# Performance work log

Hardware: AMD Instinct MI355X
Metric: run time of the kernel (lower is better)

Reference implementation:

```python
import jax, jax.numpy as jnp
import numpy as np

NCOLS = 32768   # number of independent water columns (batched)
NZ = 64         # vertical levels per column
NT = 40         # time steps
DT = 30.0       # time step [s]
GAMMA_COR = 0.55


def _edge(val, like):
    return jnp.reshape(jnp.asarray(val, like.dtype), (1,))


def add_boundaries(btm, interior, sfc):
    return jnp.concatenate([_edge(btm, interior), interior, _edge(sfc, interior)])


def tridiag_solve(a, b, c, f):
    # Thomas algorithm: forward elimination then back substitution.
    def fwd(carry, abcf):
        cp_prev, dp_prev = carry
        ai, bi, ci, fi = abcf
        denom = bi - ai * cp_prev
        cp = ci / denom
        dp = (fi - ai * dp_prev) / denom
        return (cp, dp), (cp, dp)

    zero = jnp.zeros((), a.dtype)
    _, (cp, dp) = jax.lax.scan(fwd, (zero, zero), (a, b, c, f))

    def bwd(x_next, cd):
        cpi, dpi = cd
        x = dpi - cpi * x_next
        return x, x

    _, x = jax.lax.scan(bwd, zero, (cp, dp), reverse=True)
    return x


def diffusion_solver(ak, hz, f, dt):
    a_in = -2.0 * dt * ak[1:-2] / (hz[:-2] + hz[1:-1])
    c_in = -2.0 * dt * ak[2:-1] / (hz[2:] + hz[1:-1])
    b_in = hz[1:-1] - a_in - c_in
    c_btm = -2.0 * dt * ak[1] / (hz[1] + hz[0])
    b_btm = hz[0] - c_btm
    a_sfc = -2.0 * dt * ak[-2] / (hz[-2] + hz[-1])
    b_sfc = hz[-1] - a_sfc
    a = add_boundaries(0.0, a_in, a_sfc)
    b = add_boundaries(b_btm, b_in, b_sfc)
    c = add_boundaries(c_btm, c_in, 0.0)
    return tridiag_solve(a, b, c, f)


_solve = jax.vmap(lambda ak, hz, f: diffusion_solver(ak, hz, f, DT))


def setup_inputs() -> dict:
    key = jax.random.key(0)
    ks = jax.random.split(key, 14)
    sh = (NCOLS, NZ)
    u0 = 0.1 * jax.random.normal(ks[0], sh, jnp.float32)
    v0 = 0.1 * jax.random.normal(ks[1], sh, jnp.float32)
    t0 = 15.0 + jax.random.normal(ks[2], sh, jnp.float32)
    s0 = 35.0 + 0.1 * jax.random.normal(ks[3], sh, jnp.float32)
    hz = jax.random.uniform(ks[4], sh, jnp.float32, 0.5, 2.0)
    akv = jax.random.uniform(ks[5], (NCOLS, NZ + 1), jnp.float32, 1e-4, 1e-2)
    akt = jax.random.uniform(ks[6], (NCOLS, NZ + 1), jnp.float32, 1e-4, 1e-2)
    t_forcing = 1e-5 * jax.random.normal(ks[7], sh, jnp.float32)
    s_forcing = 1e-6 * jax.random.normal(ks[8], sh, jnp.float32)
    ustr_sfc = 1e-4 * jax.random.normal(ks[9], (NCOLS,), jnp.float32)
    vstr_sfc = 1e-4 * jax.random.normal(ks[10], (NCOLS,), jnp.float32)
    ustr_btm = 1e-5 * jax.random.normal(ks[11], (NCOLS,), jnp.float32)
    vstr_btm = 1e-5 * jax.random.normal(ks[12], (NCOLS,), jnp.float32)
    fcor = jax.random.uniform(ks[13], (NCOLS,), jnp.float32, 5e-5, 1.5e-4)
    return {"u0": u0, "v0": v0, "t0": t0, "s0": s0, "hz": hz, "akv": akv,
            "akt": akt, "t_forcing": t_forcing, "s_forcing": s_forcing,
            "ustr_sfc": ustr_sfc, "vstr_sfc": vstr_sfc,
            "ustr_btm": ustr_btm, "vstr_btm": vstr_btm, "fcor": fcor}


def reference(u0, v0, t0, s0, hz, akv, akt, t_forcing, s_forcing,
              ustr_sfc, vstr_sfc, ustr_btm, vstr_btm, fcor):
    dtf = jnp.float32(DT)
    cff = (dtf * fcor) ** 2                                   # [ncols]
    cff1 = 1.0 / (1.0 + GAMMA_COR * GAMMA_COR * cff)
    coef = 1.0 - GAMMA_COR * (1.0 - GAMMA_COR) * cff
    dtfc = (dtf * fcor)[:, None]
    cff1b, coefb = cff1[:, None], coef[:, None]

    @jax.checkpoint
    def step(carry, _):
        u, v, t, s = carry
        # advance_tra_ed: tracer diffusion with constant-type forcing
        t = _solve(akt, hz, hz * t + dtf * t_forcing)
        s = _solve(akt, hz, hz * s + dtf * s_forcing)
        # advance_dyn_cor_ed: semi-implicit Coriolis + stress BCs + diffusion
        fu = cff1b * hz * (coefb * u + dtfc * v)
        fv = cff1b * hz * (coefb * v - dtfc * u)
        fu = fu.at[:, -1].add(dtf * ustr_sfc).at[:, 0].add(-dtf * ustr_btm)
        fv = fv.at[:, -1].add(dtf * vstr_sfc).at[:, 0].add(-dtf * vstr_btm)
        u = _solve(akv, hz, fu)
        v = _solve(akv, hz, fv)
        return (u, v, t, s), None

    (u, v, t, s), _ = jax.lax.scan(step, (u0, v0, t0, s0), None, length=NT)
    return jnp.stack([u, v, t, s])  # [4, ncols, nz]
```

## Files before the change

kernel.cpp:

```cpp
#include <hip/hip_runtime.h>
#include <hip/hip_bf16.h>

#define NCOLS 32768
#define NZ 64
#define NT 40
#define DTF 30.0f
#define GAMMAC 0.55f

typedef _Float16 f16;

#define SBAR() __builtin_amdgcn_sched_barrier(0)

__device__ __forceinline__ float dpp_swap1(float x) {
    return __int_as_float(__builtin_amdgcn_mov_dpp(__float_as_int(x), 0xB1, 0xF, 0xF, true));
}
__device__ __forceinline__ unsigned int packh2(float a, float b) {
    union { f16 h[2]; unsigned int u; } v;
    v.h[0] = (f16)a; v.h[1] = (f16)b; return v.u;
}
__device__ __forceinline__ unsigned short f16bits(float a) {
    union { f16 h; unsigned short u; } v; v.h = (f16)a; return v.u;
}
__device__ __forceinline__ float lo16f(unsigned int x) {
    union { unsigned int u; f16 h[2]; } v; v.u = x; return (float)v.h[0];
}
__device__ __forceinline__ float hi16f(unsigned int x) {
    union { unsigned int u; f16 h[2]; } v; v.u = x; return (float)v.h[1];
}

__global__ __launch_bounds__(256, 2) void scm_kernel(
    const float* __restrict__ u0, const float* __restrict__ v0,
    const float* __restrict__ t0, const float* __restrict__ s0,
    const float* __restrict__ hz, const float* __restrict__ akv,
    const float* __restrict__ akt, const float* __restrict__ tfo,
    const float* __restrict__ sfo, const float* __restrict__ uss,
    const float* __restrict__ vss, const float* __restrict__ usb,
    const float* __restrict__ vsb, const float* __restrict__ fcor,
    float* __restrict__ out)
{
    __shared__ uint4  Wsh[16 * 128];
    __shared__ uint4  CP4sh[8 * 128];
    __shared__ float4 P4sh[16 * 128];

    const int ltid  = threadIdx.x;
    const int tid   = blockIdx.x * 256 + ltid;
    const int field = tid & 3;
    const int col   = tid >> 2;
    const int p     = ltid >> 1;
    const bool isTS = (field >= 2);
    const int tsidx = ((ltid >> 2) << 1) | (ltid & 1);

    const float* ak  = isTS ? akt : akv;
    const float* st0 = (field == 0) ? u0 : (field == 1) ? v0 : (field == 2) ? t0 : s0;

    float walpha = 1.0f, rcor = 0.0f;
    {
        float fc   = fcor[col];
        float dtfc = DTF * fc;
        float cff  = dtfc * dtfc;
        float cff1 = 1.0f / (1.0f + GAMMAC * GAMMAC * cff);
        float coefc = 1.0f - GAMMAC * (1.0f - GAMMAC) * cff;
        if (field == 0)      { walpha = cff1 * coefc; rcor =  dtfc / coefc; }
        else if (field == 1) { walpha = cff1 * coefc; rcor = -dtfc / coefc; }
    }

    float bnd0 = 0.f, bnd63 = 0.f;
    if (field == 0)      { bnd0 = -DTF * usb[col]; bnd63 = DTF * uss[col]; }
    else if (field == 1) { bnd0 = -DTF * vsb[col]; bnd63 = DTF * vss[col]; }

    const float* hzc = hz + (size_t)col * NZ;
    const float* akc = ak + (size_t)col * (NZ + 1);
    const float* fr  = isTS ? (((field == 2) ? tfo : sfo) + (size_t)col * NZ)
                            : hzc;
    float* op = out + ((size_t)field * NCOLS + col) * NZ;

    float gb0 = 0.f, gb63 = 0.f, Sf = 0.f, Sh = 0.f;
    {
        float cpprev = 0.f, aik = 0.f, hk = hzc[0];
        uint4 wacc = {}; uint4 c8 = {};
        #pragma unroll
        for (int k = 0; k < NZ; ++k) {
            float hk1 = 0.f, aik1 = 0.f;
            float frv = fr[k];
            if (k < NZ - 1) {
                hk1  = hzc[k + 1];
                aik1 = (-2.0f * DTF) * akc[k + 1] / (hk + hk1);
            }
            Sf += DTF * frv;
            Sh += hk;
            float bk    = hk - aik - aik1;
            float denom = bk - aik * cpprev;
            float g     = 1.0f / denom;
            float cpk   = aik1 * g;
            if (k == 0)      gb0  = bnd0  * g;
            if (k == NZ - 1) gb63 = bnd63 * g;
            unsigned int   wv = packh2(hk * g * walpha, -aik * g);
            unsigned short cv = f16bits(-cpk);
            switch (k & 7) {
                case 0: wacc.x = wv; c8.x = cv; break;
                case 1: wacc.y = wv; c8.x |= ((unsigned)cv << 16); break;
                case 2: wacc.z = wv; c8.y = cv; break;
                case 3: wacc.w = wv; c8.y |= ((unsigned)cv << 16);
                        if ((ltid & 1) == 0) Wsh[(k >> 2) * 128 + p] = wacc;
                        break;
                case 4: wacc.x = wv; c8.z = cv; break;
                case 5: wacc.y = wv; c8.z |= ((unsigned)cv << 16); break;
                case 6: wacc.z = wv; c8.w = cv; break;
                default:
                    wacc.w = wv; c8.w |= ((unsigned)cv << 16);
                    if ((ltid & 1) == 0) {
                        Wsh[(k >> 2) * 128 + p]   = wacc;
                        CP4sh[(k >> 3) * 128 + p] = c8;
                    }
                    break;
            }
            cpprev = cpk; aik = aik1; hk = hk1;
            if ((k & 15) == 15) SBAR();
        }
    }
    const float mu = isTS ? (Sf / Sh) : 0.0f;

    float tau[NZ];
    {
        const float4* sp = (const float4*)(st0 + (size_t)col * NZ);
        #pragma unroll
        for (int k4 = 0; k4 < NZ / 4; ++k4) {
            float4 s = sp[k4];
            tau[4*k4+0] = s.x; tau[4*k4+1] = s.y;
            tau[4*k4+2] = s.z; tau[4*k4+3] = s.w;
        }
    }

    {
        float pv = 0.f, Pf = 0.f, Ph = 0.f;
        float4 pac;
        #pragma unroll
        for (int k = 0; k < NZ; ++k) {
            if ((k & 3) == 0) pac.x = pv;
            else if ((k & 3) == 1) pac.y = pv;
            else if ((k & 3) == 2) pac.z = pv;
            else {
                pac.w = pv;
                if (isTS) P4sh[(k >> 2) * 128 + tsidx] = pac;
            }
            if (isTS) tau[k] -= pv;
            float hk = hzc[k];
            Pf += DTF * fr[k];
            Ph += hk;
            if (k < NZ - 1) {
                float num = fmaf(-mu, Ph, Pf) * (hk + hzc[k + 1]);
                pv += num / ((-2.0f * DTF) * akc[k + 1]);
            }
            if ((k & 15) == 15) SBAR();
        }
    }

    float meanadd = 0.0f;
    if (isTS) {
        float ssum = 0.f;
        #pragma unroll
        for (int k = 0; k < NZ; ++k) ssum += tau[k];
        meanadd = ssum * (1.0f / NZ);
        #pragma unroll
        for (int k = 0; k < NZ; ++k) tau[k] -= meanadd;
    }

    __syncthreads();

    for (int n = 0; n < NT; ++n) {
        float dpprev = 0.f;
        #pragma unroll
        for (int q = 0; q < 16; ++q) {
            uint4 w = Wsh[q * 128 + p];
            #pragma unroll
            for (int i = 0; i < 4; ++i) {
                const int k = 4*q + i;
                unsigned wv = (i == 0) ? w.x : (i == 1) ? w.y
                            : (i == 2) ? w.z : w.w;
                float addend = (k == 0) ? gb0 : (k == NZ - 1) ? gb63 : 0.0f;
                float own = tau[k];
                float oth = dpp_swap1(own);
                float m   = fmaf(rcor, oth, own);
                float t   = fmaf(lo16f(wv), m, addend);
                float dp  = fmaf(hi16f(wv), dpprev, t);
                tau[k] = dp;
                dpprev = dp;
            }
            if ((q & 3) == 3) SBAR();
        }
        float xn = 0.f;
        uint4 c8;
        #pragma unroll
        for (int q = 15; q >= 0; --q) {
            if ((q & 1) == 1) c8 = CP4sh[(q >> 1) * 128 + p];
            #pragma unroll
            for (int i = 3; i >= 0; --i) {
                const int sel = ((q & 1) << 1) | (i >> 1);
                unsigned cw = (sel == 0) ? c8.x : (sel == 1) ? c8.y
                            : (sel == 2) ? c8.z : c8.w;
                float cv = (i & 1) ? hi16f(cw) : lo16f(cw);
                float x = fmaf(cv, xn, tau[4*q + i]);
                tau[4*q + i] = x;
                xn = x;
            }
            if ((q & 3) == 0) SBAR();
        }
    }

    const float base = meanadd + (float)NT * mu;
    #pragma unroll
    for (int k4 = 0; k4 < NZ / 4; ++k4) {
        float4 pv4 = make_float4(0.f, 0.f, 0.f, 0.f);
        if (isTS) pv4 = P4sh[k4 * 128 + tsidx];
        float4 w;
        w.x = tau[4*k4+0] + base + pv4.x;
        w.y = tau[4*k4+1] + base + pv4.y;
        w.z = tau[4*k4+2] + base + pv4.z;
        w.w = tau[4*k4+3] + base + pv4.w;
        ((float4*)op)[k4] = w;
    }
}

extern "C" void kernel_launch(void* const* d_in, const int* in_sizes, int n_in,
                              void* d_out, int out_size, void* d_ws, size_t ws_size,
                              hipStream_t stream) {
    const float* u0   = (const float*)d_in[0];
    const float* v0   = (const float*)d_in[1];
    const float* t0   = (const float*)d_in[2];
    const float* s0   = (const float*)d_in[3];
    const float* hz   = (const float*)d_in[4];
    const float* akv  = (const float*)d_in[5];
    const float* akt  = (const float*)d_in[6];
    const float* tfo  = (const float*)d_in[7];
    const float* sfo  = (const float*)d_in[8];
    const float* uss  = (const float*)d_in[9];
    const float* vss  = (const float*)d_in[10];
    const float* usb  = (const float*)d_in[11];
    const float* vsb  = (const float*)d_in[12];
    const float* fcor = (const float*)d_in[13];

    scm_kernel<<<dim3((NCOLS * 4) / 256), dim3(256), 0, stream>>>(
        u0, v0, t0, s0, hz, akv, akt, tfo, sfo, uss, vss, usb, vsb, fcor,
        (float*)d_out);
}
```

Before: 97.24 us.

## Fuse particular-solution pass into setup, use fast rcp and fp16 dot2 in forward sweep

Precomputes the tracer mean forcing with vectorized loads, then merges the particular-solution prefix pass into the Thomas coefficient setup loop, writing it to shared memory and subtracting it when loading initial state. Replaces IEEE divisions with hardware reciprocal approximations. In the time loop's forward elimination, packs the two operands into fp16 and uses the fdot2 instruction instead of two fmas, cutting the per-level instruction count. This lowers precision: dpprev and m are rounded to fp16, and rcp is approximate, which risks accuracy drift over 40 steps.

Result: slower. 100.0 us (+2.9%).

```diff
diff --git a/kernel.cpp b/kernel.cpp
--- a/kernel.cpp
+++ b/kernel.cpp
@@ -8,8 +8,16 @@
 #define GAMMAC 0.55f
 
 typedef _Float16 f16;
+typedef __fp16 h2v __attribute__((ext_vector_type(2)));
+
+#if __has_builtin(__builtin_amdgcn_fdot2) && __has_builtin(__builtin_amdgcn_cvt_pkrtz)
+#define HAS_DOT2 1
+#else
+#define HAS_DOT2 0
+#endif
 
 #define SBAR() __builtin_amdgcn_sched_barrier(0)
+#define RCP(x) __builtin_amdgcn_rcpf(x)
 
 __device__ __forceinline__ float dpp_swap1(float x) {
     return __int_as_float(__builtin_amdgcn_mov_dpp(__float_as_int(x), 0xB1, 0xF, 0xF, true));
@@ -26,6 +34,9 @@
 }
 __device__ __forceinline__ float hi16f(unsigned int x) {
     union { unsigned int u; f16 h[2]; } v; v.u = x; return (float)v.h[1];
+}
+__device__ __forceinline__ h2v u2h(unsigned int x) {
+    union { unsigned int u; h2v h; } v; v.u = x; return v.h;
 }
 
 __global__ __launch_bounds__(256, 2) void scm_kernel(
@@ -40,7 +51,7 @@
 {
     __shared__ uint4  Wsh[16 * 128];
     __shared__ uint4  CP4sh[8 * 128];
-    __shared__ float4 P4sh[16 * 128];
+    __shared__ float4 Psh[16 * 128];
 
     const int ltid  = threadIdx.x;
     const int tid   = blockIdx.x * 256 + ltid;
@@ -74,24 +85,46 @@
                             : hzc;
     float* op = out + ((size_t)field * NCOLS + col) * NZ;
 
-    float gb0 = 0.f, gb63 = 0.f, Sf = 0.f, Sh = 0.f;
+    float mu = 0.0f;
+    if (isTS) {
+        float sf = 0.f, sh = 0.f;
+        const float4* fp = (const float4*)fr;
+        const float4* hp = (const float4*)hzc;
+        #pragma unroll
+        for (int k4 = 0; k4 < 16; ++k4) {
+            float4 f = fp[k4], h = hp[k4];
+            sf += f.x + f.y + f.z + f.w;
+            sh += h.x + h.y + h.z + h.w;
+        }
+        mu = (DTF * sf) * RCP(sh);
+    }
+
+    float gb0 = 0.f, gb63 = 0.f;
     {
         float cpprev = 0.f, aik = 0.f, hk = hzc[0];
-        uint4 wacc = {}; uint4 c8 = {};
+        float Pf = 0.f, Ph = 0.f, pv = 0.f;
+        uint4 wacc = {}; uint4 c8 = {}; float4 pacp;
         #pragma unroll
         for (int k = 0; k < NZ; ++k) {
-            float hk1 = 0.f, aik1 = 0.f;
             float frv = fr[k];
+            if ((k & 3) == 0)      pacp.x = pv;
+            else if ((k & 3) == 1) pacp.y = pv;
+            else if ((k & 3) == 2) pacp.z = pv;
+            else {
+                pacp.w = pv;
+                if (isTS) Psh[(k >> 2) * 128 + tsidx] = pacp;
+            }
+            float hk1 = 0.f, aik1 = 0.f, rc = 0.f;
             if (k < NZ - 1) {
-                hk1  = hzc[k + 1];
-                aik1 = (-2.0f * DTF) * akc[k + 1] / (hk + hk1);
-            }
-            Sf += DTF * frv;
-            Sh += hk;
-            float bk    = hk - aik - aik1;
-            float denom = bk - aik * cpprev;
-            float g     = 1.0f / denom;
-            float cpk   = aik1 * g;
+                hk1 = hzc[k + 1];
+                float tnum = (-2.0f * DTF) * akc[k + 1];
+                float ssum = hk + hk1;
+                aik1 = tnum * RCP(ssum);
+                rc   = ssum * RCP(tnum);
+            }
+            float bk = hk - aik - aik1;
+            float g  = RCP(fmaf(-aik, cpprev, bk));
+            float cpk = aik1 * g;
             if (k == 0)      gb0  = bnd0  * g;
             if (k == NZ - 1) gb63 = bnd63 * g;
             unsigned int   wv = packh2(hk * g * walpha, -aik * g);
@@ -114,11 +147,13 @@
                     }
                     break;
             }
+            Pf += DTF * frv;
+            Ph += hk;
+            if (k < NZ - 1) pv = fmaf(fmaf(-mu, Ph, Pf), rc, pv);
             cpprev = cpk; aik = aik1; hk = hk1;
             if ((k & 15) == 15) SBAR();
         }
     }
-    const float mu = isTS ? (Sf / Sh) : 0.0f;
 
     float tau[NZ];
     {
@@ -126,32 +161,10 @@
         #pragma unroll
         for (int k4 = 0; k4 < NZ / 4; ++k4) {
             float4 s = sp[k4];
-            tau[4*k4+0] = s.x; tau[4*k4+1] = s.y;
-            tau[4*k4+2] = s.z; tau[4*k4+3] = s.w;
-        }
-    }
-
-    {
-        float pv = 0.f, Pf = 0.f, Ph = 0.f;
-        float4 pac;
-        #pragma unroll
-        for (int k = 0; k < NZ; ++k) {
-            if ((k & 3) == 0) pac.x = pv;
-            else if ((k & 3) == 1) pac.y = pv;
-            else if ((k & 3) == 2) pac.z = pv;
-            else {
-                pac.w = pv;
-                if (isTS) P4sh[(k >> 2) * 128 + tsidx] = pac;
-            }
-            if (isTS) tau[k] -= pv;
-            float hk = hzc[k];
-            Pf += DTF * fr[k];
-            Ph += hk;
-            if (k < NZ - 1) {
-                float num = fmaf(-mu, Ph, Pf) * (hk + hzc[k + 1]);
-                pv += num / ((-2.0f * DTF) * akc[k + 1]);
-            }
-            if ((k & 15) == 15) SBAR();
+            float4 pq = make_float4(0.f, 0.f, 0.f, 0.f);
+            if (isTS) pq = Psh[k4 * 128 + tsidx];
+            tau[4*k4+0] = s.x - pq.x; tau[4*k4+1] = s.y - pq.y;
+            tau[4*k4+2] = s.z - pq.z; tau[4*k4+3] = s.w - pq.w;
         }
     }
 
@@ -181,8 +194,13 @@
                 float own = tau[k];
                 float oth = dpp_swap1(own);
                 float m   = fmaf(rcor, oth, own);
-                float t   = fmaf(lo16f(wv), m, addend);
-                float dp  = fmaf(hi16f(wv), dpprev, t);
+#if HAS_DOT2
+                h2v bb = __builtin_amdgcn_cvt_pkrtz(m, dpprev);
+                float dp = __builtin_amdgcn_fdot2(u2h(wv), bb, addend, false);
+#else
+                float t1 = fmaf(lo16f(wv), m, addend);
+                float dp = fmaf(hi16f(wv), dpprev, t1);
+#endif
                 tau[k] = dp;
                 dpprev = dp;
             }
@@ -210,13 +228,13 @@
     const float base = meanadd + (float)NT * mu;
     #pragma unroll
     for (int k4 = 0; k4 < NZ / 4; ++k4) {
-        float4 pv4 = make_float4(0.f, 0.f, 0.f, 0.f);
-        if (isTS) pv4 = P4sh[k4 * 128 + tsidx];
+        float4 pq = make_float4(0.f, 0.f, 0.f, 0.f);
+        if (isTS) pq = Psh[k4 * 128 + tsidx];
         float4 w;
-        w.x = tau[4*k4+0] + base + pv4.x;
-        w.y = tau[4*k4+1] + base + pv4.y;
-        w.z = tau[4*k4+2] + base + pv4.z;
-        w.w = tau[4*k4+3] + base + pv4.w;
+        w.x = tau[4*k4+0] + base + pq.x;
+        w.y = tau[4*k4+1] + base + pq.y;
+        w.z = tau[4*k4+2] + base + pq.z;
+        w.w = tau[4*k4+3] + base + pq.w;
         ((float4*)op)[k4] = w;
     }
 }
```
